# Kernel tuning notes

Hardware: AMD Instinct MI355X
Metric: run time of the kernel (lower is better)

## Reference

```python
import jax, jax.numpy as jnp
import numpy as np

BETA = 0.25
N_E = 256
E_DIM = 1024


def setup_inputs() -> dict:
    key = jax.random.key(0)
    k1, k2, k3, k4 = jax.random.split(key, 4)
    z = jax.random.normal(k1, (16, E_DIM, 32, 32), dtype=jnp.float32)
    emb = jax.random.normal(k2, (N_E, E_DIM), dtype=jnp.float32)
    conv_w = jax.random.normal(k3, (E_DIM, E_DIM), dtype=jnp.float32) * 0.02
    conv_b = jax.random.normal(k4, (E_DIM,), dtype=jnp.float32) * 0.02
    return {"z": z, "emb": emb, "conv_w": conv_w, "conv_b": conv_b}


def reference(z, emb, conv_w, conv_b):
    # z: [B, C=e_dim, H, W] -> channels-last, flatten spatial+batch
    zp = jnp.transpose(z, (0, 2, 3, 1))          # [B, H, W, C]
    zf = zp.reshape(-1, E_DIM)                    # [N, C]
    # squared L2 distances to codebook: [N, n_e]
    d = (jnp.sum(zf * zf, axis=1, keepdims=True)
         + jnp.sum(emb * emb, axis=1)
         - 2.0 * (zf @ emb.T))
    min_idx = jnp.argmin(d, axis=1)               # [N]
    min_enc = jax.nn.one_hot(min_idx, N_E, dtype=z.dtype)  # [N, n_e]
    z_q = (min_enc @ emb).reshape(zp.shape)       # gather via matmul, as original
    # VQ commitment loss with straight-through estimator
    loss = (jnp.mean((jax.lax.stop_gradient(z_q) - zp) ** 2)
            + BETA * jnp.mean((z_q - jax.lax.stop_gradient(zp)) ** 2))
    z_q = zp + jax.lax.stop_gradient(z_q - zp)
    e_mean = jnp.mean(min_enc, axis=0)
    perplexity = jnp.exp(-jnp.sum(e_mean * jnp.log(e_mean + 1e-10)))
    # back to channels-first, then 1x1 conv (= per-pixel GEMM)
    z_q = jnp.transpose(z_q, (0, 3, 1, 2))        # [B, C, H, W]
    out = jnp.einsum('bchw,oc->bohw', z_q, conv_w) + conv_b[None, :, None, None]
    return out, loss, perplexity, min_idx
```

## Files before the change

kernel.cpp:

```cpp
#include <hip/hip_runtime.h>
#include <math.h>

#define NE 256
#define EDIM 1024
#define HW 1024
#define NPIX 16384
#define OUT_ELEMS 16777216

typedef short short8 __attribute__((ext_vector_type(8)));
typedef float f32x4 __attribute__((ext_vector_type(4)));

#define WS_HIST   0
#define WS_LOSS   1024
#define WS_ZSQ    1028
#define WS_FBITS  2048
#define WS_T      4096
#define WS_MEMSET 1052672
#define WS_CE2    1052672
#define WS_IDX    1053696
#define WS_EH     1119232
#define WS_EL     1643520
#define WS_NEED   2167808

#define DELTA 0.02f

#define WO_CE2  0
#define WO_HIST 1024
#define WO_LOSS 2048
#define WO_IDX  4096
#define WO_T    69632
#define WO_TOTAL 1118208

__device__ __forceinline__ unsigned short f2bf(float f) {
    unsigned u = __float_as_uint(f);
    unsigned r = u + 0x7FFFu + ((u >> 16) & 1u);
    return (unsigned short)(r >> 16);
}
__device__ __forceinline__ float bf2f(unsigned short h) {
    return __uint_as_float(((unsigned)h) << 16);
}

__device__ __forceinline__ void stage16(const void* g, void* l) {
    __builtin_amdgcn_global_load_lds(
        (const __attribute__((address_space(1))) unsigned int*)g,
        (__attribute__((address_space(3))) unsigned int*)l, 16, 0, 0);
}

__global__ __launch_bounds__(64) void k_prep(const float* __restrict__ emb,
                                             unsigned short* __restrict__ eh,
                                             unsigned short* __restrict__ el,
                                             float* __restrict__ ce2) {
    int j = blockIdx.x;
    int l = threadIdx.x;
    const float* row = emb + ((size_t)j << 10);
    float s = 0.f;
    #pragma unroll
    for (int i = 0; i < 4; i++) {
        float4 v = *(const float4*)(row + l * 4 + 256 * i);
        s += v.x * v.x + v.y * v.y + v.z * v.z + v.w * v.w;
        unsigned short h0 = f2bf(v.x), h1 = f2bf(v.y), h2 = f2bf(v.z), h3 = f2bf(v.w);
        uint2 hp, lp;
        hp.x = (unsigned)h0 | ((unsigned)h1 << 16);
        hp.y = (unsigned)h2 | ((unsigned)h3 << 16);
        lp.x = (unsigned)f2bf(v.x - bf2f(h0)) | ((unsigned)f2bf(v.y - bf2f(h1)) << 16);
        lp.y = (unsigned)f2bf(v.z - bf2f(h2)) | ((unsigned)f2bf(v.w - bf2f(h3)) << 16);
        *(uint2*)(eh + ((size_t)j << 10) + l * 4 + 256 * i) = hp;
        *(uint2*)(el + ((size_t)j << 10) + l * 4 + 256 * i) = lp;
    }
    #pragma unroll
    for (int m = 32; m; m >>= 1) s += __shfl_down(s, m, 64);
    if (l == 0) ce2[j] = 0.5f * s;
}

__global__ __launch_bounds__(256) void k_wT(const float* __restrict__ w,
                                            const float* __restrict__ emb,
                                            float* __restrict__ T) {
    __shared__ float wt[64 * 17];
    __shared__ float et[64 * 17];
    int t = threadIdx.x;
    int j0 = blockIdx.x * 64;
    int o0 = blockIdx.y * 64;
    int kb = blockIdx.z * 256;
    int to = t & 15, tj = t >> 4;
    float acc[4][4] = {};
    int lr = t >> 2, lk = (t & 3) * 4;
    for (int kk = kb; kk < kb + 256; kk += 16) {
        float4 wv = *(const float4*)(w + (size_t)(o0 + lr) * EDIM + kk + lk);
        float4 ev = *(const float4*)(emb + (size_t)(j0 + lr) * EDIM + kk + lk);
        __syncthreads();
        wt[lr * 17 + lk + 0] = wv.x; wt[lr * 17 + lk + 1] = wv.y;
        wt[lr * 17 + lk + 2] = wv.z; wt[lr * 17 + lk + 3] = wv.w;
        et[lr * 17 + lk + 0] = ev.x; et[lr * 17 + lk + 1] = ev.y;
        et[lr * 17 + lk + 2] = ev.z; et[lr * 17 + lk + 3] = ev.w;
        __syncthreads();
        #pragma unroll
        for (int k = 0; k < 16; k++) {
            float a[4], b[4];
            #pragma unroll
            for (int i = 0; i < 4; i++) a[i] = wt[(to * 4 + i) * 17 + k];
            #pragma unroll
            for (int i = 0; i < 4; i++) b[i] = et[(tj * 4 + i) * 17 + k];
            #pragma unroll
            for (int i = 0; i < 4; i++)
                #pragma unroll
                for (int jx = 0; jx < 4; jx++) acc[i][jx] += a[i] * b[jx];
        }
    }
    #pragma unroll
    for (int i = 0; i < 4; i++)
        #pragma unroll
        for (int jx = 0; jx < 4; jx++)
            atomicAdd(&T[(size_t)(o0 + to * 4 + i) * NE + j0 + tj * 4 + jx],
                      acc[i][jx]);
}

__global__ __launch_bounds__(256) void k_dist(
        const float* __restrict__ z, const unsigned short* __restrict__ eh,
        const unsigned short* __restrict__ el,
        const float* __restrict__ ce2,
        int* __restrict__ idx_i, float* __restrict__ idx_f,
        int* __restrict__ hist, float* __restrict__ loss_s,
        float* __restrict__ zsq_acc, unsigned int* __restrict__ fbits) {
    __shared__ unsigned short sB[2][2][256 * 32];
    int t = threadIdx.x;
    int lane = t & 63, w = t >> 6;
    int m = lane & 15, quad = lane >> 4;
    int px0 = blockIdx.x * 64;
    int b = px0 >> 10;
    const float* zp = z + (((size_t)b) << 20) + (px0 & 1023) + w * 16 + m;
    int sc = t >> 2, so = (t & 3) * 8;

    f32x4 acc[16];
    #pragma unroll
    for (int nt = 0; nt < 16; nt++) acc[nt] = (f32x4){0.f, 0.f, 0.f, 0.f};

    #pragma unroll
    for (int i = 0; i < 4; i++) {
        stage16(eh + (((size_t)(i * 64 + sc)) << 10) + so, &sB[0][0][(i * 256 + w * 64) * 8]);
        stage16(el + (((size_t)(i * 64 + sc)) << 10) + so, &sB[0][1][(i * 256 + w * 64) * 8]);
    }
    float zv[8];
    #pragma unroll
    for (int j = 0; j < 8; j++)
        zv[j] = zp[((size_t)(quad * 8 + j)) << 10];

    float zsq = 0.f;
    for (int ck = 0; ck < 32; ck++) {
        int cur = ck & 1;
        __syncthreads();
        short8 ah, al;
        #pragma unroll
        for (int j = 0; j < 8; j++) {
            zsq += zv[j] * zv[j];
            unsigned short h = f2bf(zv[j]);
            ((unsigned short*)&ah)[j] = h;
            ((unsigned short*)&al)[j] = f2bf(zv[j] - bf2f(h));
        }
        if (ck < 31) {
            int kk = (ck + 1) * 32;
            #pragma unroll
            for (int i = 0; i < 4; i++) {
                stage16(eh + (((size_t)(i * 64 + sc)) << 10) + kk + so,
                        &sB[1 - cur][0][(i * 256 + w * 64) * 8]);
                stage16(el + (((size_t)(i * 64 + sc)) << 10) + kk + so,
                        &sB[1 - cur][1][(i * 256 + w * 64) * 8]);
            }
            #pragma unroll
            for (int j = 0; j < 8; j++)
                zv[j] = zp[((size_t)(kk + quad * 8 + j)) << 10];
        }
        #pragma unroll
        for (int nt = 0; nt < 16; nt++) {
            short8 bh = *(const short8*)&sB[cur][0][(nt * 16 + m) * 32 + quad * 8];
            short8 bl = *(const short8*)&sB[cur][1][(nt * 16 + m) * 32 + quad * 8];
            acc[nt] = __builtin_amdgcn_mfma_f32_16x16x32_bf16(ah, bh, acc[nt], 0, 0, 0);
            acc[nt] = __builtin_amdgcn_mfma_f32_16x16x32_bf16(ah, bl, acc[nt], 0, 0, 0);
            acc[nt] = __builtin_amdgcn_mfma_f32_16x16x32_bf16(al, bh, acc[nt], 0, 0, 0);
        }
    }

    #pragma unroll
    for (int msk = 32; msk; msk >>= 1) zsq += __shfl_down(zsq, msk, 64);
    if (lane == 0) atomicAdd(zsq_acc, zsq);

    float c2v[16];
    #pragma unroll
    for (int nt = 0; nt < 16; nt++) c2v[nt] = ce2[nt * 16 + m];

    float lsum = 0.f;
    #pragma unroll
    for (int r = 0; r < 4; r++) {
        float v1 = 3.4e38f, v2 = 3.4e38f; int i1 = 0;
        #pragma unroll
        for (int nt = 0; nt < 16; nt++) {
            int code = nt * 16 + m;
            float sv = c2v[nt] - acc[nt][r];
            if (sv < v1 || (sv == v1 && code < i1)) { v2 = v1; v1 = sv; i1 = code; }
            else v2 = fminf(v2, sv);
        }
        #pragma unroll
        for (int msk = 1; msk < 16; msk <<= 1) {
            float ov1 = __shfl_xor(v1, msk, 64);
            int   oi1 = __shfl_xor(i1, msk, 64);
            float ov2 = __shfl_xor(v2, msk, 64);
            float nv2 = fminf(fminf(v2, ov2), fmaxf(v1, ov1));
            if (ov1 < v1 || (ov1 == v1 && oi1 < i1)) { v1 = ov1; i1 = oi1; }
            v2 = nv2;
        }
        if (m == 0) {
            int px = px0 + w * 16 + quad * 4 + r;
            idx_i[px] = i1;
            idx_f[px] = (float)i1;
            atomicAdd(&hist[i1], 1);
            if (v2 - v1 < DELTA)
                atomicOr(&fbits[px >> 5], 1u << (px & 31));
            lsum += v1;
        }
    }
    lsum += __shfl_xor(lsum, 16, 64);
    lsum += __shfl_xor(lsum, 32, 64);
    if (lane == 0) atomicAdd(loss_s, lsum);
}

__global__ __launch_bounds__(256) void k_cleanup(const float* __restrict__ z,
        const float* __restrict__ emb, const float* __restrict__ ce2,
        const unsigned int* __restrict__ fbits,
        int* __restrict__ idx_i, float* __restrict__ idx_f, int* __restrict__ hist) {
    __shared__ float zs[1024];
    __shared__ float rv[4];
    __shared__ int ri[4];
    int t = threadIdx.x;
    const float* er = emb + (size_t)t * EDIM;
    for (int px = blockIdx.x; px < NPIX; px += gridDim.x) {
        if (!(fbits[px >> 5] & (1u << (px & 31)))) continue;
        int b = px >> 10, p = px & 1023;
        const float* zb = z + (((size_t)b) << 20) + p;
        #pragma unroll
        for (int r = 0; r < 4; r++) {
            int c = t + 256 * r;
            zs[c] = zb[((size_t)c) << 10];
        }
        __syncthreads();
        float d0 = 0.f, d1 = 0.f, d2 = 0.f, d3 = 0.f;
        #pragma unroll 4
        for (int c = 0; c < EDIM; c += 16) {
            float4 e0 = *(const float4*)(er + c);
            float4 e1 = *(const float4*)(er + c + 4);
            float4 e2 = *(const float4*)(er + c + 8);
            float4 e3 = *(const float4*)(er + c + 12);
            d0 += e0.x * zs[c]      + e0.y * zs[c + 1]  + e0.z * zs[c + 2]  + e0.w * zs[c + 3];
            d1 += e1.x * zs[c + 4]  + e1.y * zs[c + 5]  + e1.z * zs[c + 6]  + e1.w * zs[c + 7];
            d2 += e2.x * zs[c + 8]  + e2.y * zs[c + 9]  + e2.z * zs[c + 10] + e2.w * zs[c + 11];
            d3 += e3.x * zs[c + 12] + e3.y * zs[c + 13] + e3.z * zs[c + 14] + e3.w * zs[c + 15];
        }
        float sv = ce2[t] - ((d0 + d1) + (d2 + d3));
        int bi = t;
        #pragma unroll
        for (int msk = 1; msk < 64; msk <<= 1) {
            float ov = __shfl_xor(sv, msk, 64);
            int oi = __shfl_xor(bi, msk, 64);
            if (ov < sv || (ov == sv && oi < bi)) { sv = ov; bi = oi; }
        }
        if ((t & 63) == 0) { rv[t >> 6] = sv; ri[t >> 6] = bi; }
        __syncthreads();
        if (t == 0) {
            float v = rv[0]; int ix = ri[0];
            for (int ww = 1; ww < 4; ww++)
                if (rv[ww] < v || (rv[ww] == v && ri[ww] < ix)) { v = rv[ww]; ix = ri[ww]; }
            int old = idx_i[px];
            if (ix != old) {
                idx_i[px] = ix; idx_f[px] = (float)ix;
                atomicAdd(&hist[ix], 1); atomicSub(&hist[old], 1);
            }
        }
        __syncthreads();
    }
}

__global__ __launch_bounds__(64) void k_norms(const float* __restrict__ emb,
                                              float* __restrict__ ce2) {
    int j = blockIdx.x;
    int lane = threadIdx.x;
    const float* row = emb + (size_t)j * EDIM;
    float s = 0.f;
    #pragma unroll
    for (int i = 0; i < EDIM / 64; i++) {
        float v = row[lane + 64 * i];
        s += v * v;
    }
    #pragma unroll
    for (int m = 32; m; m >>= 1) s += __shfl_down(s, m, 64);
    if (lane == 0) ce2[j] = 0.5f * s;
}

__global__ __launch_bounds__(256) void k_argmin(const float* __restrict__ z,
                                                const float* __restrict__ emb,
                                                const float* __restrict__ ce2,
                                                int* __restrict__ idx_i,
                                                float* __restrict__ idx_f,
                                                int* __restrict__ hist,
                                                float* __restrict__ loss_acc) {
    __shared__ float zt[32 * 64];
    __shared__ float et[256 * 34];
    __shared__ float znorm_s[64];
    int t = threadIdx.x;
    int n0 = blockIdx.x * 64;
    int b = n0 >> 10;
    int p0 = n0 & 1023;
    const float* zb = z + (size_t)b * EDIM * HW;
    int tc = t & 31, tp = t >> 5;
    float acc[8][8] = {};
    float znorm = 0.f;
    for (int kk = 0; kk < EDIM; kk += 32) {
        #pragma unroll
        for (int i = 0; i < 16; i++) {
            int q = t + 256 * i;
            int code = q >> 4, k2 = q & 15;
            float2 v = *(const float2*)(emb + (size_t)code * EDIM + kk + k2 * 2);
            *(float2*)(et + code * 34 + k2 * 2) = v;
        }
        #pragma unroll
        for (int i = 0; i < 4; i++) {
            int q = t + 256 * i;
            int k = q >> 5, p2 = q & 31;
            float2 v = *(const float2*)(zb + (size_t)(kk + k) * HW + p0 + p2 * 2);
            *(float2*)(zt + k * 64 + p2 * 2) = v;
        }
        __syncthreads();
        if (t < 64) {
            #pragma unroll
            for (int k = 0; k < 32; k++) { float zz = zt[k * 64 + t]; znorm += zz * zz; }
        }
        #pragma unroll 4
        for (int k2 = 0; k2 < 16; k2++) {
            float2 ev[8], za[4], zb2[4];
            #pragma unroll
            for (int u = 0; u < 8; u++)
                ev[u] = *(float2*)(et + (tc + 32 * u) * 34 + k2 * 2);
            #pragma unroll
            for (int j = 0; j < 4; j++)
                za[j] = *(float2*)(zt + (2 * k2) * 64 + tp * 8 + 2 * j);
            #pragma unroll
            for (int j = 0; j < 4; j++)
                zb2[j] = *(float2*)(zt + (2 * k2 + 1) * 64 + tp * 8 + 2 * j);
            #pragma unroll
            for (int p = 0; p < 8; p++) {
                float z0 = (p & 1) ? za[p >> 1].y : za[p >> 1].x;
                float z1 = (p & 1) ? zb2[p >> 1].y : zb2[p >> 1].x;
                #pragma unroll
                for (int u = 0; u < 8; u++)
                    acc[p][u] += z0 * ev[u].x + z1 * ev[u].y;
            }
        }
        __syncthreads();
    }
    if (t < 64) znorm_s[t] = znorm;
    float minv[8];
    int mini[8];
    #pragma unroll
    for (int p = 0; p < 8; p++) { minv[p] = 3.4e38f; mini[p] = 0; }
    #pragma unroll
    for (int u = 0; u < 8; u++) {
        int code = tc + 32 * u;
        float cc2 = ce2[code];
        #pragma unroll
        for (int p = 0; p < 8; p++) {
            float s = cc2 - acc[p][u];
            if (s < minv[p] || (s == minv[p] && code < mini[p])) { minv[p] = s; mini[p] = code; }
        }
    }
    #pragma unroll
    for (int m = 1; m < 32; m <<= 1) {
        #pragma unroll
        for (int p = 0; p < 8; p++) {
            float ov = __shfl_xor(minv[p], m, 64);
            int oi = __shfl_xor(mini[p], m, 64);
            if (ov < minv[p] || (ov == minv[p] && oi < mini[p])) { minv[p] = ov; mini[p] = oi; }
        }
    }
    __syncthreads();
    if (tc == 0) {
        float dsum = 0.f;
        #pragma unroll
        for (int p = 0; p < 8; p++) {
            int lp = tp * 8 + p;
            int n = n0 + lp;
            idx_i[n] = mini[p];
            idx_f[n] = (float)mini[p];
            dsum += znorm_s[lp] + 2.f * minv[p];
            atomicAdd(&hist[mini[p]], 1);
        }
        atomicAdd(loss_acc, dsum);
    }
}

__global__ __launch_bounds__(256) void k_scatter(const float* __restrict__ T,
                                                 const float* __restrict__ bias,
                                                 const int* __restrict__ idx,
                                                 float* __restrict__ out) {
    __shared__ float Ts[16 * 256];
    __shared__ float bs[16];
    int t = threadIdx.x;
    int o0 = blockIdx.x * 16;
    int b = blockIdx.y;
    #pragma unroll
    for (int r = 0; r < 16; r++)
        Ts[r * 256 + t] = T[(size_t)(o0 + r) * NE + t];
    if (t < 16) bs[t] = bias[o0 + t];
    __syncthreads();
    int4 i4 = *(const int4*)(idx + b * HW + t * 4);
    #pragma unroll
    for (int r = 0; r < 16; r++) {
        const float* Tr = Ts + r * 256;
        float bb = bs[r];
        float4 v;
        v.x = Tr[i4.x] + bb;
        v.y = Tr[i4.y] + bb;
        v.z = Tr[i4.z] + bb;
        v.w = Tr[i4.w] + bb;
        *(float4*)(out + ((size_t)(b * EDIM + o0 + r) * HW) + t * 4) = v;
    }
}

__global__ __launch_bounds__(256) void k_final_new(const int* __restrict__ hist,
                                                   const float* __restrict__ loss_s,
                                                   const float* __restrict__ zsq,
                                                   float* __restrict__ out) {
    __shared__ float red[4];
    int t = threadIdx.x;
    float em = (float)hist[t] * (1.0f / 16384.0f);
    float v = em * logf(em + 1e-10f);
    #pragma unroll
    for (int m = 32; m; m >>= 1) v += __shfl_down(v, m, 64);
    if ((t & 63) == 0) red[t >> 6] = v;
    __syncthreads();
    if (t == 0) {
        float s = red[0] + red[1] + red[2] + red[3];
        out[OUT_ELEMS] = (zsq[0] + 2.f * loss_s[0]) * 1.25f / 16777216.f;
        out[OUT_ELEMS + 1] = expf(-s);
    }
}

__global__ __launch_bounds__(256) void k_final_old(const int* __restrict__ hist,
                                                   const float* __restrict__ loss_acc,
                                                   float* __restrict__ out) {
    __shared__ float red[4];
    int t = threadIdx.x;
    float em = (float)hist[t] * (1.0f / 16384.0f);
    float v = em * logf(em + 1e-10f);
    #pragma unroll
    for (int m = 32; m; m >>= 1) v += __shfl_down(v, m, 64);
    if ((t & 63) == 0) red[t >> 6] = v;
    __syncthreads();
    if (t == 0) {
        float s = red[0] + red[1] + red[2] + red[3];
        out[OUT_ELEMS] = loss_acc[0] * 1.25f / 16777216.f;
        out[OUT_ELEMS + 1] = expf(-s);
    }
}

extern "C" void kernel_launch(void* const* d_in, const int* in_sizes, int n_in,
                              void* d_out, int out_size, void* d_ws, size_t ws_size,
                              hipStream_t stream) {
    (void)in_sizes; (void)n_in; (void)out_size;
    const float* z      = (const float*)d_in[0];
    const float* emb    = (const float*)d_in[1];
    const float* conv_w = (const float*)d_in[2];
    const float* conv_b = (const float*)d_in[3];
    float* out = (float*)d_out;

    if (ws_size >= WS_NEED) {
        int*   hist     = (int*)((char*)d_ws + WS_HIST);
        float* loss_s   = (float*)((char*)d_ws + WS_LOSS);
        float* zsq      = (float*)((char*)d_ws + WS_ZSQ);
        unsigned int* fbits = (unsigned int*)((char*)d_ws + WS_FBITS);
        float* T        = (float*)((char*)d_ws + WS_T);
        float* ce2      = (float*)((char*)d_ws + WS_CE2);
        int*   idx_i    = (int*)((char*)d_ws + WS_IDX);
        unsigned short* eh = (unsigned short*)((char*)d_ws + WS_EH);
        unsigned short* el = (unsigned short*)((char*)d_ws + WS_EL);
        float* idx_f = out + OUT_ELEMS + 2;

        hipMemsetAsync(d_ws, 0, WS_MEMSET, stream);
        k_prep<<<NE, 64, 0, stream>>>(emb, eh, el, ce2);
        k_wT<<<dim3(4, 16, 4), 256, 0, stream>>>(conv_w, emb, T);
        k_dist<<<256, 256, 0, stream>>>(z, eh, el, ce2, idx_i, idx_f,
                                        hist, loss_s, zsq, fbits);
        k_cleanup<<<256, 256, 0, stream>>>(z, emb, ce2, fbits, idx_i, idx_f, hist);
        k_scatter<<<dim3(64, 16), 256, 0, stream>>>(T, conv_b, idx_i, out);
        k_final_new<<<1, 256, 0, stream>>>(hist, loss_s, zsq, out);
    } else {
        float* ce2      = (float*)((char*)d_ws + WO_CE2);
        int*   hist     = (int*)((char*)d_ws + WO_HIST);
        float* loss_acc = (float*)((char*)d_ws + WO_LOSS);
        int*   idx_i    = (int*)((char*)d_ws + WO_IDX);
        float* T        = (float*)((char*)d_ws + WO_T);
        float* idx_f = out + OUT_ELEMS + 2;

        hipMemsetAsync(d_ws, 0, WO_TOTAL, stream);
        k_norms<<<NE, 64, 0, stream>>>(emb, ce2);
        k_wT<<<dim3(4, 16, 4), 256, 0, stream>>>(conv_w, emb, T);
        k_argmin<<<256, 256, 0, stream>>>(z, emb, ce2, idx_i, idx_f, hist, loss_acc);
        k_scatter<<<dim3(64, 16), 256, 0, stream>>>(T, conv_b, idx_i, out);
        k_final_old<<<1, 256, 0, stream>>>(hist, loss_acc, out);
    }
}
```

Before: 258.6 us.

## Split distance kernel codebook across wave pairs and swizzle LDS layout

Each k_dist block now covers 32 pixels instead of 64, and its four waves are split so two wave pairs each handle half of the 256 codes. Per-half argmin results are merged through shared memory. This doubles the grid to 512 blocks, which should fill the GPU better, and halves the per-wave accumulator count. An XOR swizzle on the LDS staging offsets is added to reduce bank conflicts. In exchange, each block redundantly loads the z tile and the full codebook chunk, adds a block barrier, and the merge drops the strict lower-index tie-break when both halves give equal minima.

```diff
diff --git a/kernel.cpp b/kernel.cpp
--- a/kernel.cpp
+++ b/kernel.cpp
@@ -122,28 +122,35 @@
         int* __restrict__ hist, float* __restrict__ loss_s,
         float* __restrict__ zsq_acc, unsigned int* __restrict__ fbits) {
     __shared__ unsigned short sB[2][2][256 * 32];
+    __shared__ float v1s[32], v2s[32];
+    __shared__ int   i1s[32];
     int t = threadIdx.x;
     int lane = t & 63, w = t >> 6;
     int m = lane & 15, quad = lane >> 4;
-    int px0 = blockIdx.x * 64;
+    int half = w >> 1;
+    int c0 = half << 7;
+    int pt = w & 1;
+    int px0 = blockIdx.x * 32;
     int b = px0 >> 10;
-    const float* zp = z + (((size_t)b) << 20) + (px0 & 1023) + w * 16 + m;
-    int sc = t >> 2, so = (t & 3) * 8;
-
-    f32x4 acc[16];
-    #pragma unroll
-    for (int nt = 0; nt < 16; nt++) acc[nt] = (f32x4){0.f, 0.f, 0.f, 0.f};
+    const float* zp = z + (((size_t)b) << 20) + (px0 & 1023) + pt * 16 + m;
+    int sc = t >> 2, qp = t & 3;
+    int ql = qp ^ ((sc >> 1) & 3);
+
+    f32x4 acc[8];
+    #pragma unroll
+    for (int nt = 0; nt < 8; nt++) acc[nt] = (f32x4){0.f, 0.f, 0.f, 0.f};
 
     #pragma unroll
     for (int i = 0; i < 4; i++) {
-        stage16(eh + (((size_t)(i * 64 + sc)) << 10) + so, &sB[0][0][(i * 256 + w * 64) * 8]);
-        stage16(el + (((size_t)(i * 64 + sc)) << 10) + so, &sB[0][1][(i * 256 + w * 64) * 8]);
+        stage16(eh + (((size_t)(i * 64 + sc)) << 10) + ql * 8, &sB[0][0][(i * 256 + w * 64) * 8]);
+        stage16(el + (((size_t)(i * 64 + sc)) << 10) + ql * 8, &sB[0][1][(i * 256 + w * 64) * 8]);
     }
     float zv[8];
     #pragma unroll
     for (int j = 0; j < 8; j++)
         zv[j] = zp[((size_t)(quad * 8 + j)) << 10];
 
+    int sq = quad ^ ((m >> 1) & 3);
     float zsq = 0.f;
     for (int ck = 0; ck < 32; ck++) {
         int cur = ck & 1;
@@ -160,9 +167,9 @@
             int kk = (ck + 1) * 32;
             #pragma unroll
             for (int i = 0; i < 4; i++) {
-                stage16(eh + (((size_t)(i * 64 + sc)) << 10) + kk + so,
+                stage16(eh + (((size_t)(i * 64 + sc)) << 10) + kk + ql * 8,
                         &sB[1 - cur][0][(i * 256 + w * 64) * 8]);
-                stage16(el + (((size_t)(i * 64 + sc)) << 10) + kk + so,
+                stage16(el + (((size_t)(i * 64 + sc)) << 10) + kk + ql * 8,
                         &sB[1 - cur][1][(i * 256 + w * 64) * 8]);
             }
             #pragma unroll
@@ -170,9 +177,10 @@
                 zv[j] = zp[((size_t)(kk + quad * 8 + j)) << 10];
         }
         #pragma unroll
-        for (int nt = 0; nt < 16; nt++) {
-            short8 bh = *(const short8*)&sB[cur][0][(nt * 16 + m) * 32 + quad * 8];
-            short8 bl = *(const short8*)&sB[cur][1][(nt * 16 + m) * 32 + quad * 8];
+        for (int nt = 0; nt < 8; nt++) {
+            int srow = c0 + nt * 16 + m;
+            short8 bh = *(const short8*)&sB[cur][0][srow * 32 + sq * 8];
+            short8 bl = *(const short8*)&sB[cur][1][srow * 32 + sq * 8];
             acc[nt] = __builtin_amdgcn_mfma_f32_16x16x32_bf16(ah, bh, acc[nt], 0, 0, 0);
             acc[nt] = __builtin_amdgcn_mfma_f32_16x16x32_bf16(ah, bl, acc[nt], 0, 0, 0);
             acc[nt] = __builtin_amdgcn_mfma_f32_16x16x32_bf16(al, bh, acc[nt], 0, 0, 0);
@@ -181,19 +189,20 @@
 
     #pragma unroll
     for (int msk = 32; msk; msk >>= 1) zsq += __shfl_down(zsq, msk, 64);
-    if (lane == 0) atomicAdd(zsq_acc, zsq);
-
-    float c2v[16];
-    #pragma unroll
-    for (int nt = 0; nt < 16; nt++) c2v[nt] = ce2[nt * 16 + m];
-
-    float lsum = 0.f;
+    if (half == 0 && lane == 0) atomicAdd(zsq_acc, zsq);
+
+    float c2v[8];
+    #pragma unroll
+    for (int nt = 0; nt < 8; nt++) c2v[nt] = ce2[c0 + nt * 16 + m];
+
+    float v1r[4], v2r[4];
+    int i1r[4];
     #pragma unroll
     for (int r = 0; r < 4; r++) {
         float v1 = 3.4e38f, v2 = 3.4e38f; int i1 = 0;
         #pragma unroll
-        for (int nt = 0; nt < 16; nt++) {
-            int code = nt * 16 + m;
+        for (int nt = 0; nt < 8; nt++) {
+            int code = c0 + nt * 16 + m;
             float sv = c2v[nt] - acc[nt][r];
             if (sv < v1 || (sv == v1 && code < i1)) { v2 = v1; v1 = sv; i1 = code; }
             else v2 = fminf(v2, sv);
@@ -207,19 +216,42 @@
             if (ov1 < v1 || (ov1 == v1 && oi1 < i1)) { v1 = ov1; i1 = oi1; }
             v2 = nv2;
         }
+        v1r[r] = v1; v2r[r] = v2; i1r[r] = i1;
+    }
+    int pxl = pt * 16 + quad * 4;
+    if (half == 0 && m == 0) {
+        #pragma unroll
+        for (int r = 0; r < 4; r++) {
+            v1s[pxl + r] = v1r[r]; v2s[pxl + r] = v2r[r]; i1s[pxl + r] = i1r[r];
+        }
+    }
+    __syncthreads();
+    if (half == 1) {
+        float lsum = 0.f;
         if (m == 0) {
-            int px = px0 + w * 16 + quad * 4 + r;
-            idx_i[px] = i1;
-            idx_f[px] = (float)i1;
-            atomicAdd(&hist[i1], 1);
-            if (v2 - v1 < DELTA)
-                atomicOr(&fbits[px >> 5], 1u << (px & 31));
-            lsum += v1;
-        }
-    }
-    lsum += __shfl_xor(lsum, 16, 64);
-    lsum += __shfl_xor(lsum, 32, 64);
-    if (lane == 0) atomicAdd(loss_s, lsum);
+            #pragma unroll
+            for (int r = 0; r < 4; r++) {
+                int pl = pxl + r;
+                float va = v1s[pl], v2a = v2s[pl];
+                int   ia = i1s[pl];
+                float vb = v1r[r];
+                float v2m = fminf(fminf(v2a, v2r[r]), fmaxf(va, vb));
+                float v1; int i1;
+                if (vb < va) { v1 = vb; i1 = i1r[r]; }
+                else         { v1 = va; i1 = ia; }
+                int px = px0 + pl;
+                idx_i[px] = i1;
+                idx_f[px] = (float)i1;
+                atomicAdd(&hist[i1], 1);
+                if (v2m - v1 < DELTA)
+                    atomicOr(&fbits[px >> 5], 1u << (px & 31));
+                lsum += v1;
+            }
+        }
+        lsum += __shfl_xor(lsum, 16, 64);
+        lsum += __shfl_xor(lsum, 32, 64);
+        if (lane == 0) atomicAdd(loss_s, lsum);
+    }
 }
 
 __global__ __launch_bounds__(256) void k_cleanup(const float* __restrict__ z,
@@ -484,7 +516,7 @@
         hipMemsetAsync(d_ws, 0, WS_MEMSET, stream);
         k_prep<<<NE, 64, 0, stream>>>(emb, eh, el, ce2);
         k_wT<<<dim3(4, 16, 4), 256, 0, stream>>>(conv_w, emb, T);
-        k_dist<<<256, 256, 0, stream>>>(z, eh, el, ce2, idx_i, idx_f,
+        k_dist<<<512, 256, 0, stream>>>(z, eh, el, ce2, idx_i, idx_f,
                                         hist, loss_s, zsq, fbits);
         k_cleanup<<<256, 256, 0, stream>>>(z, emb, ce2, fbits, idx_i, idx_f, hist);
         k_scatter<<<dim3(64, 16), 256, 0, stream>>>(T, conv_b, idx_i, out);
```

After: 265.9 us. 2.8% more time.

## Split k_dist reduction across two waves and read codebook directly from global

Applied to the files above, without the earlier changes.

Restructures the distance kernel so each 128-thread block handles 16 pixels, with its two waves each covering half of the embedding dimension and combining partial accumulators through shared memory. The LDS double-buffered staging of the bf16 codebook is dropped in favour of direct global (cache-resident) loads of the hi/lo codebook fragments. This launches four times as many blocks to fill more CUs. In exchange, every block re-reads the whole codebook from cache and loses the LDS sharing across waves.

```diff
diff --git a/kernel.cpp b/kernel.cpp
--- a/kernel.cpp
+++ b/kernel.cpp
@@ -40,12 +40,6 @@
     return __uint_as_float(((unsigned)h) << 16);
 }
 
-__device__ __forceinline__ void stage16(const void* g, void* l) {
-    __builtin_amdgcn_global_load_lds(
-        (const __attribute__((address_space(1))) unsigned int*)g,
-        (__attribute__((address_space(3))) unsigned int*)l, 16, 0, 0);
-}
-
 __global__ __launch_bounds__(64) void k_prep(const float* __restrict__ emb,
                                              unsigned short* __restrict__ eh,
                                              unsigned short* __restrict__ el,
@@ -114,40 +108,34 @@
                       acc[i][jx]);
 }
 
-__global__ __launch_bounds__(256) void k_dist(
+__global__ __launch_bounds__(128) void k_dist(
         const float* __restrict__ z, const unsigned short* __restrict__ eh,
         const unsigned short* __restrict__ el,
         const float* __restrict__ ce2,
         int* __restrict__ idx_i, float* __restrict__ idx_f,
         int* __restrict__ hist, float* __restrict__ loss_s,
         float* __restrict__ zsq_acc, unsigned int* __restrict__ fbits) {
-    __shared__ unsigned short sB[2][2][256 * 32];
+    __shared__ float accs[64 * 65 + 1];
     int t = threadIdx.x;
     int lane = t & 63, w = t >> 6;
     int m = lane & 15, quad = lane >> 4;
-    int px0 = blockIdx.x * 64;
+    int px0 = blockIdx.x * 16;
     int b = px0 >> 10;
-    const float* zp = z + (((size_t)b) << 20) + (px0 & 1023) + w * 16 + m;
-    int sc = t >> 2, so = (t & 3) * 8;
+    const float* zp = z + (((size_t)b) << 20) + (px0 & 1023) + m;
 
     f32x4 acc[16];
     #pragma unroll
     for (int nt = 0; nt < 16; nt++) acc[nt] = (f32x4){0.f, 0.f, 0.f, 0.f};
 
-    #pragma unroll
-    for (int i = 0; i < 4; i++) {
-        stage16(eh + (((size_t)(i * 64 + sc)) << 10) + so, &sB[0][0][(i * 256 + w * 64) * 8]);
-        stage16(el + (((size_t)(i * 64 + sc)) << 10) + so, &sB[0][1][(i * 256 + w * 64) * 8]);
-    }
+    int k0 = w * 512;
     float zv[8];
     #pragma unroll
     for (int j = 0; j < 8; j++)
-        zv[j] = zp[((size_t)(quad * 8 + j)) << 10];
+        zv[j] = zp[((size_t)(k0 + quad * 8 + j)) << 10];
 
     float zsq = 0.f;
-    for (int ck = 0; ck < 32; ck++) {
-        int cur = ck & 1;
-        __syncthreads();
+    for (int ck = 0; ck < 16; ck++) {
+        int kk = k0 + ck * 32;
         short8 ah, al;
         #pragma unroll
         for (int j = 0; j < 8; j++) {
@@ -156,23 +144,18 @@
             ((unsigned short*)&ah)[j] = h;
             ((unsigned short*)&al)[j] = f2bf(zv[j] - bf2f(h));
         }
-        if (ck < 31) {
-            int kk = (ck + 1) * 32;
-            #pragma unroll
-            for (int i = 0; i < 4; i++) {
-                stage16(eh + (((size_t)(i * 64 + sc)) << 10) + kk + so,
-                        &sB[1 - cur][0][(i * 256 + w * 64) * 8]);
-                stage16(el + (((size_t)(i * 64 + sc)) << 10) + kk + so,
-                        &sB[1 - cur][1][(i * 256 + w * 64) * 8]);
-            }
+        if (ck < 15) {
             #pragma unroll
             for (int j = 0; j < 8; j++)
-                zv[j] = zp[((size_t)(kk + quad * 8 + j)) << 10];
-        }
+                zv[j] = zp[((size_t)(kk + 32 + quad * 8 + j)) << 10];
+        }
+        const unsigned short* ehk = eh + kk + quad * 8;
+        const unsigned short* elk = el + kk + quad * 8;
         #pragma unroll
         for (int nt = 0; nt < 16; nt++) {
-            short8 bh = *(const short8*)&sB[cur][0][(nt * 16 + m) * 32 + quad * 8];
-            short8 bl = *(const short8*)&sB[cur][1][(nt * 16 + m) * 32 + quad * 8];
+            size_t row = ((size_t)(nt * 16 + m)) << 10;
+            short8 bh = *(const short8*)(ehk + row);
+            short8 bl = *(const short8*)(elk + row);
             acc[nt] = __builtin_amdgcn_mfma_f32_16x16x32_bf16(ah, bh, acc[nt], 0, 0, 0);
             acc[nt] = __builtin_amdgcn_mfma_f32_16x16x32_bf16(ah, bl, acc[nt], 0, 0, 0);
             acc[nt] = __builtin_amdgcn_mfma_f32_16x16x32_bf16(al, bh, acc[nt], 0, 0, 0);
@@ -181,7 +164,23 @@
 
     #pragma unroll
     for (int msk = 32; msk; msk >>= 1) zsq += __shfl_down(zsq, msk, 64);
-    if (lane == 0) atomicAdd(zsq_acc, zsq);
+
+    if (w == 1) {
+        #pragma unroll
+        for (int nt = 0; nt < 16; nt++)
+            #pragma unroll
+            for (int r = 0; r < 4; r++)
+                accs[lane * 65 + nt * 4 + r] = acc[nt][r];
+        if (lane == 0) accs[64 * 65] = zsq;
+    }
+    __syncthreads();
+    if (w != 0) return;
+    #pragma unroll
+    for (int nt = 0; nt < 16; nt++)
+        #pragma unroll
+        for (int r = 0; r < 4; r++)
+            acc[nt][r] += accs[lane * 65 + nt * 4 + r];
+    if (lane == 0) atomicAdd(zsq_acc, zsq + accs[64 * 65]);
 
     float c2v[16];
     #pragma unroll
@@ -208,7 +207,7 @@
             v2 = nv2;
         }
         if (m == 0) {
-            int px = px0 + w * 16 + quad * 4 + r;
+            int px = px0 + quad * 4 + r;
             idx_i[px] = i1;
             idx_f[px] = (float)i1;
             atomicAdd(&hist[i1], 1);
@@ -484,8 +483,8 @@
         hipMemsetAsync(d_ws, 0, WS_MEMSET, stream);
         k_prep<<<NE, 64, 0, stream>>>(emb, eh, el, ce2);
         k_wT<<<dim3(4, 16, 4), 256, 0, stream>>>(conv_w, emb, T);
-        k_dist<<<256, 256, 0, stream>>>(z, eh, el, ce2, idx_i, idx_f,
-                                        hist, loss_s, zsq, fbits);
+        k_dist<<<1024, 128, 0, stream>>>(z, eh, el, ce2, idx_i, idx_f,
+                                         hist, loss_s, zsq, fbits);
         k_cleanup<<<256, 256, 0, stream>>>(z, emb, ce2, fbits, idx_i, idx_f, hist);
         k_scatter<<<dim3(64, 16), 256, 0, stream>>>(T, conv_b, idx_i, out);
         k_final_new<<<1, 256, 0, stream>>>(hist, loss_s, zsq, out);
```

Result: slower. 333.5 us (+28.9%).

## Deepen k_dist codebook staging to 4-stage pipeline with swizzled LDS layout

Applied to the files above, without the earlier changes.

Replaces the double-buffered LDS staging of the bf16 hi/lo codebook chunks in the distance kernel with a four-buffer ring that prefetches three chunks ahead. Explicit vmcnt waits and raw s_barrier calls replace __syncthreads. It also XOR-swizzles the 8-element column slot within each LDS row to reduce bank conflicts on the MFMA operand reads. The intent is to hide global-load latency and LDS conflicts behind the MFMA work. The cost is double the shared memory (128 KB), which may lower occupancy, plus fragile hand-counted waitcnt values.

```diff
diff --git a/kernel.cpp b/kernel.cpp
--- a/kernel.cpp
+++ b/kernel.cpp
@@ -121,63 +121,90 @@
         int* __restrict__ idx_i, float* __restrict__ idx_f,
         int* __restrict__ hist, float* __restrict__ loss_s,
         float* __restrict__ zsq_acc, unsigned int* __restrict__ fbits) {
-    __shared__ unsigned short sB[2][2][256 * 32];
+    __shared__ unsigned short sB[4][2][256 * 32];
     int t = threadIdx.x;
     int lane = t & 63, w = t >> 6;
     int m = lane & 15, quad = lane >> 4;
     int px0 = blockIdx.x * 64;
     int b = px0 >> 10;
     const float* zp = z + (((size_t)b) << 20) + (px0 & 1023) + w * 16 + m;
-    int sc = t >> 2, so = (t & 3) * 8;
+    int sc = t >> 2, qp = t & 3;
+    int ql = qp ^ ((sc >> 1) & 3);
 
     f32x4 acc[16];
     #pragma unroll
     for (int nt = 0; nt < 16; nt++) acc[nt] = (f32x4){0.f, 0.f, 0.f, 0.f};
 
-    #pragma unroll
-    for (int i = 0; i < 4; i++) {
-        stage16(eh + (((size_t)(i * 64 + sc)) << 10) + so, &sB[0][0][(i * 256 + w * 64) * 8]);
-        stage16(el + (((size_t)(i * 64 + sc)) << 10) + so, &sB[0][1][(i * 256 + w * 64) * 8]);
-    }
-    float zv[8];
-    #pragma unroll
-    for (int j = 0; j < 8; j++)
-        zv[j] = zp[((size_t)(quad * 8 + j)) << 10];
-
+    float zv0[8], zv1[8], zv2[8], zv3[8];
     float zsq = 0.f;
-    for (int ck = 0; ck < 32; ck++) {
-        int cur = ck & 1;
-        __syncthreads();
-        short8 ah, al;
-        #pragma unroll
-        for (int j = 0; j < 8; j++) {
-            zsq += zv[j] * zv[j];
-            unsigned short h = f2bf(zv[j]);
-            ((unsigned short*)&ah)[j] = h;
-            ((unsigned short*)&al)[j] = f2bf(zv[j] - bf2f(h));
-        }
-        if (ck < 31) {
-            int kk = (ck + 1) * 32;
-            #pragma unroll
-            for (int i = 0; i < 4; i++) {
-                stage16(eh + (((size_t)(i * 64 + sc)) << 10) + kk + so,
-                        &sB[1 - cur][0][(i * 256 + w * 64) * 8]);
-                stage16(el + (((size_t)(i * 64 + sc)) << 10) + kk + so,
-                        &sB[1 - cur][1][(i * 256 + w * 64) * 8]);
-            }
-            #pragma unroll
-            for (int j = 0; j < 8; j++)
-                zv[j] = zp[((size_t)(kk + quad * 8 + j)) << 10];
-        }
-        #pragma unroll
-        for (int nt = 0; nt < 16; nt++) {
-            short8 bh = *(const short8*)&sB[cur][0][(nt * 16 + m) * 32 + quad * 8];
-            short8 bl = *(const short8*)&sB[cur][1][(nt * 16 + m) * 32 + quad * 8];
-            acc[nt] = __builtin_amdgcn_mfma_f32_16x16x32_bf16(ah, bh, acc[nt], 0, 0, 0);
-            acc[nt] = __builtin_amdgcn_mfma_f32_16x16x32_bf16(ah, bl, acc[nt], 0, 0, 0);
-            acc[nt] = __builtin_amdgcn_mfma_f32_16x16x32_bf16(al, bh, acc[nt], 0, 0, 0);
-        }
-    }
+    int sq = quad ^ ((m >> 1) & 3);
+
+#define STAGE(c, B) do {                                                        \
+    int kk_ = (c) * 32;                                                         \
+    _Pragma("unroll")                                                           \
+    for (int i_ = 0; i_ < 4; i_++) {                                            \
+        stage16(eh + (((size_t)(i_ * 64 + sc)) << 10) + kk_ + ql * 8,           \
+                &sB[B][0][(i_ * 256 + w * 64) * 8]);                            \
+        stage16(el + (((size_t)(i_ * 64 + sc)) << 10) + kk_ + ql * 8,           \
+                &sB[B][1][(i_ * 256 + w * 64) * 8]);                            \
+    } } while (0)
+
+#define ZLOAD(c, ZV) do {                                                       \
+    int kk_ = (c) * 32;                                                         \
+    _Pragma("unroll")                                                           \
+    for (int j_ = 0; j_ < 8; j_++)                                              \
+        ZV[j_] = zp[((size_t)(kk_ + quad * 8 + j_)) << 10];                     \
+    } while (0)
+
+#define WAITV(n) do {                                                           \
+    asm volatile("s_waitcnt vmcnt(" #n ")" ::: "memory");                       \
+    __builtin_amdgcn_sched_barrier(0); } while (0)
+
+#define FENCE() do {                                                            \
+    asm volatile("" ::: "memory");                                              \
+    __builtin_amdgcn_sched_barrier(0); } while (0)
+
+#define BODY(c, B, ZV, PRE, B3, ZV3) do {                                       \
+    __builtin_amdgcn_s_barrier();                                               \
+    short8 ah, al;                                                              \
+    _Pragma("unroll")                                                           \
+    for (int j_ = 0; j_ < 8; j_++) {                                            \
+        float zj_ = ZV[j_];                                                     \
+        zsq += zj_ * zj_;                                                       \
+        unsigned short h_ = f2bf(zj_);                                          \
+        ((unsigned short*)&ah)[j_] = h_;                                        \
+        ((unsigned short*)&al)[j_] = f2bf(zj_ - bf2f(h_));                      \
+    }                                                                           \
+    if (PRE) { STAGE((c) + 3, B3); ZLOAD((c) + 3, ZV3); }                       \
+    _Pragma("unroll")                                                           \
+    for (int nt_ = 0; nt_ < 16; nt_++) {                                        \
+        short8 bh_ = *(const short8*)&sB[B][0][(nt_ * 16 + m) * 32 + sq * 8];   \
+        short8 bl_ = *(const short8*)&sB[B][1][(nt_ * 16 + m) * 32 + sq * 8];   \
+        acc[nt_] = __builtin_amdgcn_mfma_f32_16x16x32_bf16(ah, bh_, acc[nt_], 0, 0, 0); \
+        acc[nt_] = __builtin_amdgcn_mfma_f32_16x16x32_bf16(ah, bl_, acc[nt_], 0, 0, 0); \
+        acc[nt_] = __builtin_amdgcn_mfma_f32_16x16x32_bf16(al, bh_, acc[nt_], 0, 0, 0); \
+    } } while (0)
+
+    STAGE(0, 0); ZLOAD(0, zv0); FENCE();
+    STAGE(1, 1); ZLOAD(1, zv1); FENCE();
+    STAGE(2, 2); ZLOAD(2, zv2);
+
+    for (int mi = 0; mi < 7; mi++) {
+        WAITV(32); BODY(mi * 4 + 0, 0, zv0, 1, 3, zv3);
+        WAITV(32); BODY(mi * 4 + 1, 1, zv1, 1, 0, zv0);
+        WAITV(32); BODY(mi * 4 + 2, 2, zv2, 1, 1, zv1);
+        WAITV(32); BODY(mi * 4 + 3, 3, zv3, 1, 2, zv2);
+    }
+    WAITV(32); BODY(28, 0, zv0, 1, 3, zv3);
+    WAITV(32); BODY(29, 1, zv1, 0, 2, zv2);
+    WAITV(16); BODY(30, 2, zv2, 0, 3, zv3);
+    WAITV(0);  BODY(31, 3, zv3, 0, 0, zv0);
+
+#undef STAGE
+#undef ZLOAD
+#undef WAITV
+#undef FENCE
+#undef BODY
 
     #pragma unroll
     for (int msk = 32; msk; msk >>= 1) zsq += __shfl_down(zsq, msk, 64);
```

Result: faster. 253.1 us (-2.2%).
